# Optimization experiments

Hardware: AMD Instinct MI355X
Metric: run time of the kernel (lower is better)

Reference implementation:

```python
import jax, jax.numpy as jnp
import numpy as np

NUM_HEADS = 12
HIDDEN = 768
HEAD_DIM = HIDDEN // NUM_HEADS  # 64
B, S = 2, 2048


def setup_inputs() -> dict:
    key = jax.random.key(0)
    ks = jax.random.split(key, 8)
    inp = {
        "hidden_states": jax.random.normal(ks[0], (B, S, HIDDEN), dtype=jnp.float32),
        "attention_mask": jnp.zeros((B, 1, 1, S), dtype=jnp.float32),
        "Wq": jax.random.normal(ks[1], (HIDDEN, HIDDEN), dtype=jnp.float32) * 0.02,
        "bq": jnp.zeros((HIDDEN,), dtype=jnp.float32),
        "Wk": jax.random.normal(ks[2], (HIDDEN, HIDDEN), dtype=jnp.float32) * 0.02,
        "bk": jnp.zeros((HIDDEN,), dtype=jnp.float32),
        "Wv": jax.random.normal(ks[3], (HIDDEN, HIDDEN), dtype=jnp.float32) * 0.02,
        "bv": jnp.zeros((HIDDEN,), dtype=jnp.float32),
    }
    return inp


def _split_heads(x):
    # [B, S, H*d] -> [B, H, S, d]
    b, s, _ = x.shape
    return x.reshape(b, s, NUM_HEADS, HEAD_DIM).transpose(0, 2, 1, 3)


def reference(hidden_states, attention_mask, Wq, bq, Wk, bk, Wv, bv):
    # Q/K/V projections (nn.Linear: x @ W.T + b; W generated square so direct matmul is equivalent math)
    q = _split_heads(hidden_states @ Wq + bq)  # [B,H,S,d]
    k = _split_heads(hidden_states @ Wk + bk)
    v = _split_heads(hidden_states @ Wv + bv)

    scale = 1.0 / np.sqrt(HEAD_DIM).astype(np.float32)
    scores = jnp.einsum("bhqd,bhkd->bhqk", q, k) * scale  # [B,H,S,S]
    scores = scores + attention_mask  # additive mask, broadcast [B,1,1,S]
    probs = jax.nn.softmax(scores, axis=-1)
    # dropout prob = 0.0 -> identity (eval mode)
    ctx = jnp.einsum("bhqk,bhkd->bhqd", probs, v)  # [B,H,S,d]
    ctx = ctx.transpose(0, 2, 1, 3).reshape(hidden_states.shape[0], hidden_states.shape[1], HIDDEN)
    return ctx
```

## Files before the change

### kernel.cpp

```cpp
#include <hip/hip_runtime.h>

#define S_LEN 2048
#define HID   768
#define NH    12
#define HD    64
#define BATCH 2
#define GK    768
#define L2E   1.44269504088896340736f

typedef __attribute__((ext_vector_type(8))) short bf16x8;
typedef __attribute__((ext_vector_type(4))) float f32x4;
typedef __attribute__((ext_vector_type(4))) short s16x4;
typedef __attribute__((ext_vector_type(8))) short s16x8;

__device__ __forceinline__ unsigned short f2bf(float f) {
    union { float f; unsigned int u; } v; v.f = f;
    unsigned int r = v.u + 0x7fffu + ((v.u >> 16) & 1u);
    return (unsigned short)(r >> 16);
}

__global__ __launch_bounds__(256) void prep_kernel(
    const float* __restrict__ X, const float* __restrict__ Wq,
    const float* __restrict__ Wk, const float* __restrict__ Wv,
    unsigned short* __restrict__ Xb, unsigned short* __restrict__ Wt) {
    __shared__ float T[32][33];
    int bid = blockIdx.x;
    if (bid < 3072) {
        int id = bid * 256 + threadIdx.x;
        float4 v = ((const float4*)X)[id];
        s16x4 o; o[0] = (short)f2bf(v.x); o[1] = (short)f2bf(v.y);
        o[2] = (short)f2bf(v.z); o[3] = (short)f2bf(v.w);
        ((s16x4*)Xb)[id] = o;
        return;
    }
    int t2 = bid - 3072;
    int mat = t2 / 576, t = t2 % 576;
    int tk = t / 24, tn = t % 24;
    const float* W = (mat == 0) ? Wq : (mat == 1) ? Wk : Wv;
    int r  = threadIdx.x >> 3;
    int c4 = (threadIdx.x & 7) * 4;
    float4 v = *(const float4*)&W[(size_t)(tk*32 + r) * GK + tn*32 + c4];
    T[c4+0][r] = v.x; T[c4+1][r] = v.y; T[c4+2][r] = v.z; T[c4+3][r] = v.w;
    __syncthreads();
    s16x4 o;
    o[0] = (short)f2bf(T[r][c4+0]); o[1] = (short)f2bf(T[r][c4+1]);
    o[2] = (short)f2bf(T[r][c4+2]); o[3] = (short)f2bf(T[r][c4+3]);
    *(s16x4*)&Wt[(size_t)(mat*768 + tn*32 + r) * GK + tk*32 + c4] = o;
}

__global__ __launch_bounds__(256) void gemm_qkv(
    const unsigned short* __restrict__ Xb, const unsigned short* __restrict__ Wt,
    const float* __restrict__ bq, const float* __restrict__ bk,
    const float* __restrict__ bv,
    unsigned short* __restrict__ qb, unsigned short* __restrict__ kb,
    unsigned short* __restrict__ vb) {
    __shared__ __align__(16) unsigned short As[128][72];
    __shared__ __align__(16) unsigned short Bs[64][72];

    const int tid = threadIdx.x;
    const int bm = blockIdx.y * 128;
    const int bn = blockIdx.x * 64;
    const int w = tid >> 6, l = tid & 63, quad = l >> 4, lq = l & 15;
    const int wx = w & 1, wy = w >> 1;

    f32x4 zero = {0.f, 0.f, 0.f, 0.f};
    f32x4 acc[4][2];
#pragma unroll
    for (int mi = 0; mi < 4; mi++)
#pragma unroll
        for (int ni = 0; ni < 2; ni++) acc[mi][ni] = zero;

    for (int k0 = 0; k0 < GK; k0 += 64) {
        __syncthreads();
#pragma unroll
        for (int i = 0; i < 4; i++) {
            int id = i * 256 + tid;
            int row = id >> 3, k8 = (id & 7) * 8;
            *(s16x8*)&As[row][k8] = *(const s16x8*)&Xb[(size_t)(bm + row) * GK + k0 + k8];
        }
#pragma unroll
        for (int i = 0; i < 2; i++) {
            int id = i * 256 + tid;
            int row = id >> 3, k8 = (id & 7) * 8;
            *(s16x8*)&Bs[row][k8] = *(const s16x8*)&Wt[(size_t)(bn + row) * GK + k0 + k8];
        }
        __syncthreads();
#pragma unroll
        for (int kh = 0; kh < 2; kh++) {
            bf16x8 a[4], b[2];
#pragma unroll
            for (int mi = 0; mi < 4; mi++)
                a[mi] = *(const bf16x8*)&As[wy*64 + mi*16 + lq][kh*32 + quad*8];
#pragma unroll
            for (int ni = 0; ni < 2; ni++)
                b[ni] = *(const bf16x8*)&Bs[wx*32 + ni*16 + lq][kh*32 + quad*8];
#pragma unroll
            for (int mi = 0; mi < 4; mi++)
#pragma unroll
                for (int ni = 0; ni < 2; ni++)
                    acc[mi][ni] = __builtin_amdgcn_mfma_f32_16x16x32_bf16(
                        a[mi], b[ni], acc[mi][ni], 0, 0, 0);
        }
    }

    const int mat = bn / 768;
    const float* bias = (mat == 0) ? bq : (mat == 1) ? bk : bv;
    const float scl = (mat == 0) ? 0.125f * L2E : 1.0f;
    const int nbase = bn % 768;
#pragma unroll
    for (int ni = 0; ni < 2; ni++) {
        int hn = nbase + wx*32 + ni*16 + lq;
        float bval = bias[hn];
        int h = hn >> 6, d = hn & 63;
#pragma unroll
        for (int mi = 0; mi < 4; mi++) {
            int m0 = bm + wy*64 + mi*16 + quad*4;
            int b_ = m0 >> 11, s0 = m0 & 2047;
            if (mat == 2) {
                s16x4 pk;
#pragma unroll
                for (int r = 0; r < 4; r++) pk[r] = (short)f2bf(acc[mi][ni][r] + bval);
                *(s16x4*)&vb[((size_t)((b_*NH + h) * HD + d)) * S_LEN + s0] = pk;
            } else {
                unsigned short* outp = (mat == 0) ? qb : kb;
#pragma unroll
                for (int r = 0; r < 4; r++) {
                    float v = (acc[mi][ni][r] + bval) * scl;
                    outp[((size_t)((b_*NH + h) * S_LEN + s0 + r)) * HD + d] = f2bf(v);
                }
            }
        }
    }
}

__global__ __launch_bounds__(256) void attn_kernel(
    const unsigned short* __restrict__ Qg, const unsigned short* __restrict__ Kg,
    const unsigned short* __restrict__ Vtg, const float* __restrict__ maskg,
    float* __restrict__ out) {
    __shared__ __align__(16) unsigned short Ks[2][64][72];
    __shared__ __align__(16) unsigned short Vt[2][64][72];
    __shared__ __align__(16) unsigned short Ps[4][16][72];

    const int tid = threadIdx.x;
    const int w = tid >> 6, l = tid & 63, quad = l >> 4, lq = l & 15;
    const int bh = blockIdx.y;
    const int q0 = blockIdx.x * 64;
    const int bi = bh / NH, hi = bh % NH;
    const unsigned short* Kh = Kg + (size_t)bh * S_LEN * HD;
    const unsigned short* Vh = Vtg + (size_t)bh * HD * S_LEN;
    const float* mb = maskg + (size_t)bi * S_LEN;

    const int srow = tid >> 3;
    const int sc8  = (tid & 7) * 8;

    const unsigned short* Qrow = Qg + ((size_t)bh * S_LEN + q0 + w*16 + lq) * HD;
    const bf16x8 a0 = *(const bf16x8*)&Qrow[quad*8];
    const bf16x8 a1 = *(const bf16x8*)&Qrow[32 + quad*8];

    bf16x8 ones;
#pragma unroll
    for (int i = 0; i < 8; i++) ones[i] = (short)0x3F80;

    f32x4 zero = {0.f, 0.f, 0.f, 0.f};
    f32x4 o[4], lsum = zero;
#pragma unroll
    for (int ng = 0; ng < 4; ng++) o[ng] = zero;

#pragma unroll
    for (int i = 0; i < 2; i++) {
        int row = srow + i*32;
        *(s16x8*)&Ks[0][row][sc8] = *(const s16x8*)&Kh[(size_t)row * HD + sc8];
        *(s16x8*)&Vt[0][row][sc8] = *(const s16x8*)&Vh[(size_t)row * S_LEN + sc8];
    }
    __syncthreads();

    for (int kt = 0; kt < S_LEN / 64; kt++) {
        const int cur = kt & 1;
        if (kt + 1 < S_LEN / 64) {
            const int kn = (kt + 1) * 64;
#pragma unroll
            for (int i = 0; i < 2; i++) {
                int row = srow + i*32;
                *(s16x8*)&Ks[cur^1][row][sc8] = *(const s16x8*)&Kh[(size_t)(kn + row) * HD + sc8];
                *(s16x8*)&Vt[cur^1][row][sc8] = *(const s16x8*)&Vh[(size_t)row * S_LEN + kn + sc8];
            }
        }

        const int kk = kt * 64;
        float mm[4];
#pragma unroll
        for (int g = 0; g < 4; g++) mm[g] = mb[kk + g*16 + lq] * L2E;

        f32x4 s[4];
#pragma unroll
        for (int g = 0; g < 4; g++) {
            bf16x8 b0 = *(const bf16x8*)&Ks[cur][g*16 + lq][quad*8];
            bf16x8 b1 = *(const bf16x8*)&Ks[cur][g*16 + lq][32 + quad*8];
            f32x4 z = __builtin_amdgcn_mfma_f32_16x16x32_bf16(a0, b0, zero, 0, 0, 0);
            s[g]    = __builtin_amdgcn_mfma_f32_16x16x32_bf16(a1, b1, z,    0, 0, 0);
        }

#pragma unroll
        for (int g = 0; g < 4; g++)
#pragma unroll
            for (int r = 0; r < 4; r++) {
                float p = exp2f(s[g][r] + mm[g]);
                Ps[w][quad*4 + r][g*16 + lq] = f2bf(p);
            }

        bf16x8 pa0 = *(const bf16x8*)&Ps[w][lq][quad*8];
        bf16x8 pa1 = *(const bf16x8*)&Ps[w][lq][32 + quad*8];

        lsum = __builtin_amdgcn_mfma_f32_16x16x32_bf16(pa0, ones, lsum, 0, 0, 0);
        lsum = __builtin_amdgcn_mfma_f32_16x16x32_bf16(pa1, ones, lsum, 0, 0, 0);

#pragma unroll
        for (int ng = 0; ng < 4; ng++) {
            bf16x8 v0 = *(const bf16x8*)&Vt[cur][ng*16 + lq][quad*8];
            bf16x8 v1 = *(const bf16x8*)&Vt[cur][ng*16 + lq][32 + quad*8];
            f32x4 t = __builtin_amdgcn_mfma_f32_16x16x32_bf16(pa0, v0, o[ng], 0, 0, 0);
            o[ng]   = __builtin_amdgcn_mfma_f32_16x16x32_bf16(pa1, v1, t,     0, 0, 0);
        }

        __syncthreads();
    }

#pragma unroll
    for (int r = 0; r < 4; r++) {
        const float inv = 1.0f / lsum[r];
        const int row = q0 + w*16 + quad*4 + r;
#pragma unroll
        for (int ng = 0; ng < 4; ng++)
            out[((size_t)(bi * S_LEN + row)) * HID + hi*HD + ng*16 + lq] = o[ng][r] * inv;
    }
}

extern "C" void kernel_launch(void* const* d_in, const int* in_sizes, int n_in,
                              void* d_out, int out_size, void* d_ws, size_t ws_size,
                              hipStream_t stream) {
    const float* X    = (const float*)d_in[0];
    const float* mask = (const float*)d_in[1];
    const float* Wq   = (const float*)d_in[2];
    const float* bq   = (const float*)d_in[3];
    const float* Wk   = (const float*)d_in[4];
    const float* bk   = (const float*)d_in[5];
    const float* Wv   = (const float*)d_in[6];
    const float* bv   = (const float*)d_in[7];
    float* out = (float*)d_out;

    const size_t per = (size_t)BATCH * NH * S_LEN * HD;
    unsigned short* qb = (unsigned short*)d_ws;
    unsigned short* kb = qb + per;
    unsigned short* vb = kb + per;
    unsigned short* xb = vb + per;
    unsigned short* wt = xb + (size_t)4096 * GK;

    prep_kernel<<<4800, 256, 0, stream>>>(X, Wq, Wk, Wv, xb, wt);

    dim3 ggrid(2304 / 64, 4096 / 128);
    gemm_qkv<<<ggrid, 256, 0, stream>>>(xb, wt, bq, bk, bv, qb, kb, vb);

    dim3 agrid(S_LEN / 64, BATCH * NH);
    attn_kernel<<<agrid, 256, 0, stream>>>(qb, kb, vb, mask, out);
}
```

Measured before the change: 174.8 us.

## Use direct global-to-LDS loads for GEMM and attention K/V staging

Replaces the register-staged global→shared copies in the QKV GEMM and the attention K/V double buffer with global_load_lds 16-byte direct-to-LDS transfers. The LDS padding is dropped so each wave writes contiguous rows, and the attention loop is unrolled by two with fixed buffer indices. This removes VGPR round trips and the address math for staging. The price is unpadded LDS rows, which can cause bank conflicts on the MFMA operand reads, and reliance on s_waitcnt handling for the async loads at the barriers.

```diff
diff --git a/kernel.cpp b/kernel.cpp
--- a/kernel.cpp
+++ b/kernel.cpp
@@ -18,6 +18,10 @@
     unsigned int r = v.u + 0x7fffu + ((v.u >> 16) & 1u);
     return (unsigned short)(r >> 16);
 }
+
+#define GLL16(gp, lp) __builtin_amdgcn_global_load_lds( \
+    (const __attribute__((address_space(1))) unsigned int*)(gp), \
+    (__attribute__((address_space(3))) unsigned int*)(lp), 16, 0, 0)
 
 __global__ __launch_bounds__(256) void prep_kernel(
     const float* __restrict__ X, const float* __restrict__ Wq,
@@ -54,8 +58,8 @@
     const float* __restrict__ bv,
     unsigned short* __restrict__ qb, unsigned short* __restrict__ kb,
     unsigned short* __restrict__ vb) {
-    __shared__ __align__(16) unsigned short As[128][72];
-    __shared__ __align__(16) unsigned short Bs[64][72];
+    __shared__ __align__(16) unsigned short As[128][64];
+    __shared__ __align__(16) unsigned short Bs[64][64];
 
     const int tid = threadIdx.x;
     const int bm = blockIdx.y * 128;
@@ -63,6 +67,9 @@
     const int w = tid >> 6, l = tid & 63, quad = l >> 4, lq = l & 15;
     const int wx = w & 1, wy = w >> 1;
 
+    const unsigned short* aga = Xb + (size_t)(bm + w*32 + (l >> 3)) * GK + (l & 7) * 8;
+    const unsigned short* bga = Wt + (size_t)(bn + w*16 + (l >> 3)) * GK + (l & 7) * 8;
+
     f32x4 zero = {0.f, 0.f, 0.f, 0.f};
     f32x4 acc[4][2];
 #pragma unroll
@@ -73,17 +80,11 @@
     for (int k0 = 0; k0 < GK; k0 += 64) {
         __syncthreads();
 #pragma unroll
-        for (int i = 0; i < 4; i++) {
-            int id = i * 256 + tid;
-            int row = id >> 3, k8 = (id & 7) * 8;
-            *(s16x8*)&As[row][k8] = *(const s16x8*)&Xb[(size_t)(bm + row) * GK + k0 + k8];
-        }
-#pragma unroll
-        for (int i = 0; i < 2; i++) {
-            int id = i * 256 + tid;
-            int row = id >> 3, k8 = (id & 7) * 8;
-            *(s16x8*)&Bs[row][k8] = *(const s16x8*)&Wt[(size_t)(bn + row) * GK + k0 + k8];
-        }
+        for (int i = 0; i < 4; i++)
+            GLL16(aga + k0 + i*8*GK, &As[w*32 + i*8][0]);
+#pragma unroll
+        for (int i = 0; i < 2; i++)
+            GLL16(bga + k0 + i*8*GK, &Bs[w*16 + i*8][0]);
         __syncthreads();
 #pragma unroll
         for (int kh = 0; kh < 2; kh++) {
@@ -123,11 +124,10 @@
                 *(s16x4*)&vb[((size_t)((b_*NH + h) * HD + d)) * S_LEN + s0] = pk;
             } else {
                 unsigned short* outp = (mat == 0) ? qb : kb;
-#pragma unroll
-                for (int r = 0; r < 4; r++) {
-                    float v = (acc[mi][ni][r] + bval) * scl;
-                    outp[((size_t)((b_*NH + h) * S_LEN + s0 + r)) * HD + d] = f2bf(v);
-                }
+                size_t base = ((size_t)((b_*NH + h) * S_LEN + s0)) * HD + d;
+#pragma unroll
+                for (int r = 0; r < 4; r++)
+                    outp[base + (size_t)r * HD] = f2bf((acc[mi][ni][r] + bval) * scl);
             }
         }
     }
@@ -137,8 +137,8 @@
     const unsigned short* __restrict__ Qg, const unsigned short* __restrict__ Kg,
     const unsigned short* __restrict__ Vtg, const float* __restrict__ maskg,
     float* __restrict__ out) {
-    __shared__ __align__(16) unsigned short Ks[2][64][72];
-    __shared__ __align__(16) unsigned short Vt[2][64][72];
+    __shared__ __align__(16) unsigned short Ks[2][64][64];
+    __shared__ __align__(16) unsigned short Vt[2][64][64];
     __shared__ __align__(16) unsigned short Ps[4][16][72];
 
     const int tid = threadIdx.x;
@@ -150,9 +150,6 @@
     const unsigned short* Vh = Vtg + (size_t)bh * HD * S_LEN;
     const float* mb = maskg + (size_t)bi * S_LEN;
 
-    const int srow = tid >> 3;
-    const int sc8  = (tid & 7) * 8;
-
     const unsigned short* Qrow = Qg + ((size_t)bh * S_LEN + q0 + w*16 + lq) * HD;
     const bf16x8 a0 = *(const bf16x8*)&Qrow[quad*8];
     const bf16x8 a1 = *(const bf16x8*)&Qrow[32 + quad*8];
@@ -161,31 +158,23 @@
 #pragma unroll
     for (int i = 0; i < 8; i++) ones[i] = (short)0x3F80;
 
+    const unsigned short* kga = Kh + (size_t)(w*16 + (l >> 3)) * HD + (l & 7) * 8;
+    const unsigned short* vga = Vh + (size_t)(w*16 + (l >> 3)) * S_LEN + (l & 7) * 8;
+
     f32x4 zero = {0.f, 0.f, 0.f, 0.f};
     f32x4 o[4], lsum = zero;
 #pragma unroll
     for (int ng = 0; ng < 4; ng++) o[ng] = zero;
 
-#pragma unroll
-    for (int i = 0; i < 2; i++) {
-        int row = srow + i*32;
-        *(s16x8*)&Ks[0][row][sc8] = *(const s16x8*)&Kh[(size_t)row * HD + sc8];
-        *(s16x8*)&Vt[0][row][sc8] = *(const s16x8*)&Vh[(size_t)row * S_LEN + sc8];
-    }
-    __syncthreads();
-
-    for (int kt = 0; kt < S_LEN / 64; kt++) {
-        const int cur = kt & 1;
-        if (kt + 1 < S_LEN / 64) {
-            const int kn = (kt + 1) * 64;
-#pragma unroll
-            for (int i = 0; i < 2; i++) {
-                int row = srow + i*32;
-                *(s16x8*)&Ks[cur^1][row][sc8] = *(const s16x8*)&Kh[(size_t)(kn + row) * HD + sc8];
-                *(s16x8*)&Vt[cur^1][row][sc8] = *(const s16x8*)&Vh[(size_t)row * S_LEN + kn + sc8];
-            }
-        }
-
+    auto stage = [&](int buf, int kt) {
+#pragma unroll
+        for (int i = 0; i < 2; i++) {
+            GLL16(kga + (size_t)kt*64*HD + i*8*HD, &Ks[buf][w*16 + i*8][0]);
+            GLL16(vga + kt*64 + (size_t)i*8*S_LEN, &Vt[buf][w*16 + i*8][0]);
+        }
+    };
+
+    auto compute = [&](int buf, int kt) {
         const int kk = kt * 64;
         float mm[4];
 #pragma unroll
@@ -194,19 +183,19 @@
         f32x4 s[4];
 #pragma unroll
         for (int g = 0; g < 4; g++) {
-            bf16x8 b0 = *(const bf16x8*)&Ks[cur][g*16 + lq][quad*8];
-            bf16x8 b1 = *(const bf16x8*)&Ks[cur][g*16 + lq][32 + quad*8];
+            bf16x8 b0 = *(const bf16x8*)&Ks[buf][g*16 + lq][quad*8];
+            bf16x8 b1 = *(const bf16x8*)&Ks[buf][g*16 + lq][32 + quad*8];
             f32x4 z = __builtin_amdgcn_mfma_f32_16x16x32_bf16(a0, b0, zero, 0, 0, 0);
             s[g]    = __builtin_amdgcn_mfma_f32_16x16x32_bf16(a1, b1, z,    0, 0, 0);
         }
 
 #pragma unroll
-        for (int g = 0; g < 4; g++)
-#pragma unroll
-            for (int r = 0; r < 4; r++) {
-                float p = exp2f(s[g][r] + mm[g]);
-                Ps[w][quad*4 + r][g*16 + lq] = f2bf(p);
-            }
+        for (int g = 0; g < 4; g++) {
+            const int col = g*16 + lq;
+#pragma unroll
+            for (int r = 0; r < 4; r++)
+                Ps[w][quad*4 + r][col] = f2bf(exp2f(s[g][r] + mm[g]));
+        }
 
         bf16x8 pa0 = *(const bf16x8*)&Ps[w][lq][quad*8];
         bf16x8 pa1 = *(const bf16x8*)&Ps[w][lq][32 + quad*8];
@@ -216,12 +205,22 @@
 
 #pragma unroll
         for (int ng = 0; ng < 4; ng++) {
-            bf16x8 v0 = *(const bf16x8*)&Vt[cur][ng*16 + lq][quad*8];
-            bf16x8 v1 = *(const bf16x8*)&Vt[cur][ng*16 + lq][32 + quad*8];
+            bf16x8 v0 = *(const bf16x8*)&Vt[buf][ng*16 + lq][quad*8];
+            bf16x8 v1 = *(const bf16x8*)&Vt[buf][ng*16 + lq][32 + quad*8];
             f32x4 t = __builtin_amdgcn_mfma_f32_16x16x32_bf16(pa0, v0, o[ng], 0, 0, 0);
             o[ng]   = __builtin_amdgcn_mfma_f32_16x16x32_bf16(pa1, v1, t,     0, 0, 0);
         }
-
+    };
+
+    stage(0, 0);
+    __syncthreads();
+
+    for (int kt = 0; kt < S_LEN / 64; kt += 2) {
+        stage(1, kt + 1);
+        compute(0, kt);
+        __syncthreads();
+        if (kt + 2 < S_LEN / 64) stage(0, kt + 2);
+        compute(1, kt + 1);
         __syncthreads();
     }
 
```

New measurement: 182.5 us. 1.04x slower.
